# Optimization experiments

Hardware: AMD Instinct MI355X
Metric: run time of the kernel (lower is better)

## Reference

```python
import jax, jax.numpy as jnp
from jax import lax
import numpy as np

SEQ_LEN, INPUT_DIM, HID, NCLS, BATCH = 1024, 1, 512, 10, 256


def setup_inputs() -> dict:
    key = jax.random.key(0)
    k1, k2, k3, k4 = jax.random.split(key, 4)
    def xavier(k, shape):
        fan_in, fan_out = shape[1], shape[0]
        bound = np.sqrt(6.0 / (fan_in + fan_out))
        return jax.random.uniform(k, shape, jnp.float32, -bound, bound)
    return {
        "x": jax.random.normal(k1, (BATCH, SEQ_LEN), jnp.float32),
        "h_init": jnp.zeros((HID, 1), jnp.float32),
        "W_hx": xavier(k2, (HID, INPUT_DIM)),
        "W_hh": xavier(k3, (HID, HID)),
        "b_h": jnp.zeros((HID, 1), jnp.float32),
        "W_ph": xavier(k4, (NCLS, HID)),
        "b_p": jnp.zeros((NCLS, 1), jnp.float32),
    }


def reference(x, h_init, W_hx, W_hh, b_h, W_ph, b_p):
    # x: [B, T] scalar inputs per step (input_dim == 1)
    B = x.shape[0]
    H = h_init.shape[0]
    # Broadcasting h_init [H,1] to [H,B] up-front is mathematically identical
    # to the torch code (W_hh @ h_init broadcasts against [H,B] at step 0).
    h0 = jnp.broadcast_to(h_init, (H, B))

    def step(h, x_t):
        # x_t: [B]; W_hx @ x_t[None,:] -> [H, B]
        h_new = jnp.tanh(W_hx @ x_t[None, :] + W_hh @ h + b_h)
        return h_new, None

    h_last, _ = lax.scan(step, h0, x.T)  # scan over time axis [T, B]
    p = W_ph @ h_last + b_p  # [NCLS, B]
    return p.T  # [B, NCLS]
```

## Files before the change

kernel.cpp:

```cpp
#include <hip/hip_runtime.h>


#define T_SEQ    1024
#define HID      512
#define NTHREADS 512
#define NW       8
#define NCLS     10
#define RP       8
#define PAIRS    32
#define PREG     28
#define PSTRIDE  576

typedef _Float16 half2_t __attribute__((ext_vector_type(2)));

__device__ __forceinline__ unsigned int pack2(float a, float b) {
    half2_t h = {(_Float16)a, (_Float16)b};
    return __builtin_bit_cast(unsigned int, h);
}

__device__ __forceinline__ float dot2(unsigned int w, unsigned int h, float acc) {
#if __has_builtin(__builtin_amdgcn_fdot2)
    return __builtin_amdgcn_fdot2(__builtin_bit_cast(half2_t, w),
                                  __builtin_bit_cast(half2_t, h), acc, false);
#else
    half2_t wv = __builtin_bit_cast(half2_t, w), hv = __builtin_bit_cast(half2_t, h);
    return acc + (float)wv.x * (float)hv.x + (float)wv.y * (float)hv.y;
#endif
}

__device__ __forceinline__ unsigned int bcast(unsigned int v, int lane) {
#if __has_builtin(__builtin_amdgcn_readlane)
    return __builtin_amdgcn_readlane(v, lane);
#else
    return __shfl((int)v, lane, 64);
#endif
}

__device__ __forceinline__ int pidx(int row) { return row + ((row >> 5) << 2); }

__device__ __forceinline__ float fast_tanh(float s) {
#if __has_builtin(__builtin_amdgcn_exp2f)
    float e = __builtin_amdgcn_exp2f(s * 2.885390081777927f);
#else
    float e = __expf(2.0f * s);
#endif
    return 1.0f - 2.0f / (e + 1.0f);
}

__global__ __attribute__((amdgpu_flat_work_group_size(NTHREADS, NTHREADS)))
           __attribute__((amdgpu_waves_per_eu(2, 2)))
void rnn_persist(
    const float* __restrict__ x, const float* __restrict__ h_init,
    const float* __restrict__ W_hx, const float* __restrict__ W_hh,
    const float* __restrict__ b_h, const float* __restrict__ W_ph,
    const float* __restrict__ b_p, float* __restrict__ out)
{
    __shared__ uint4    Wl4[NW * RP * 64];
    __shared__ float    part[2][NW][PSTRIDE];
    __shared__ float    x_s[T_SEQ];
    __shared__ _Float16 hs[HID];

    const int tid  = threadIdx.x;
    const int b    = blockIdx.x;
    const int w    = tid >> 6;
    const int lane = tid & 63;

    for (int i = tid; i < T_SEQ; i += NTHREADS) x_s[i] = x[(size_t)b * T_SEQ + i];

    const float whx = W_hx[tid];
    const float bh  = b_h[tid];
    const int   pi  = pidx(tid);
    hs[tid] = (_Float16)h_init[tid];

    unsigned int wreg[RP][PREG];
    #pragma unroll
    for (int r = 0; r < RP; ++r) {
        const float4* row = (const float4*)(W_hh + (size_t)(RP * lane + r) * HID + 64 * w);
        #pragma unroll
        for (int q = 0; q < 7; ++q) {
            float4 v = row[q];
            wreg[r][2 * q]     = pack2(v.x, v.y);
            wreg[r][2 * q + 1] = pack2(v.z, v.w);
        }
#if __has_builtin(__builtin_amdgcn_sched_barrier)
        __builtin_amdgcn_sched_barrier(0);
#endif
        #pragma unroll
        for (int q = 7; q < 14; ++q) {
            float4 v = row[q];
            wreg[r][2 * q]     = pack2(v.x, v.y);
            wreg[r][2 * q + 1] = pack2(v.z, v.w);
        }
        float4 v14 = row[14], v15 = row[15];
        Wl4[(w * RP + r) * 64 + lane] =
            make_uint4(pack2(v14.x, v14.y), pack2(v14.z, v14.w),
                       pack2(v15.x, v15.y), pack2(v15.z, v15.w));
#if __has_builtin(__builtin_amdgcn_sched_barrier)
        __builtin_amdgcn_sched_barrier(0);
#endif
    }

    #pragma unroll
    for (int r = 0; r < RP; ++r)
        #pragma unroll
        for (int p = 0; p < PREG; ++p)
            asm volatile("" : "+v"(wreg[r][p]));

    __syncthreads();

    const unsigned int* hs32 = (const unsigned int*)hs;
    float hval = 0.0f;

    #pragma unroll 1
    for (int t = 0; t < T_SEQ; ++t) {
        const int buf = t & 1;
        const float xw = x_s[t];

        unsigned int hpack = hs32[w * 32 + (lane & 31)];

        float acc[RP];
        #pragma unroll
        for (int r = 0; r < RP; ++r) acc[r] = 0.0f;

        #pragma unroll
        for (int p = 0; p < PREG; ++p) {
            unsigned int hp = bcast(hpack, p);
            #pragma unroll
            for (int r = 0; r < RP; ++r) acc[r] = dot2(wreg[r][p], hp, acc[r]);
        }
        {
            unsigned int hh0 = bcast(hpack, 28), hh1 = bcast(hpack, 29),
                         hh2 = bcast(hpack, 30), hh3 = bcast(hpack, 31);
            #pragma unroll
            for (int r = 0; r < RP; ++r) {
                uint4 wq = Wl4[(w * RP + r) * 64 + lane];
                acc[r] = dot2(wq.x, hh0, acc[r]);
                acc[r] = dot2(wq.y, hh1, acc[r]);
                acc[r] = dot2(wq.z, hh2, acc[r]);
                acc[r] = dot2(wq.w, hh3, acc[r]);
            }
        }

        *(float4*)&part[buf][w][pidx(RP * lane)]     = make_float4(acc[0], acc[1], acc[2], acc[3]);
        *(float4*)&part[buf][w][pidx(RP * lane + 4)] = make_float4(acc[4], acc[5], acc[6], acc[7]);

        __syncthreads();

        float s = whx * xw + bh;
        #pragma unroll
        for (int j = 0; j < NW; ++j) s += part[buf][j][pi];

        hval = fast_tanh(s);
        hs[tid] = (_Float16)hval;
    }

    __syncthreads();
    x_s[tid] = hval;
    __syncthreads();

    for (int c = w; c < NCLS; c += NW) {
        float s = 0.0f;
        #pragma unroll
        for (int j = 0; j < 8; ++j) {
            int r = lane + 64 * j;
            s += W_ph[c * HID + r] * x_s[r];
        }
        #pragma unroll
        for (int off = 32; off; off >>= 1) s += __shfl_down(s, off, 64);
        if (lane == 0) out[b * NCLS + c] = s + b_p[c];
    }
}

extern "C" void kernel_launch(void* const* d_in, const int* in_sizes, int n_in,
                              void* d_out, int out_size, void* d_ws, size_t ws_size,
                              hipStream_t stream) {
    const float* x      = (const float*)d_in[0];
    const float* h_init = (const float*)d_in[1];
    const float* W_hx   = (const float*)d_in[2];
    const float* W_hh   = (const float*)d_in[3];
    const float* b_h    = (const float*)d_in[4];
    const float* W_ph   = (const float*)d_in[5];
    const float* b_p    = (const float*)d_in[6];
    float* out = (float*)d_out;

    const int B = in_sizes[0] / T_SEQ;
    rnn_persist<<<B, NTHREADS, 0, stream>>>(x, h_init, W_hx, W_hh, b_h, W_ph, b_p, out);
}
```

Before: 1.436 ms.

## Keep packed hidden state in registers, removing LDS h round-trip per step

Each lane now computes the two hidden rows that its wave will broadcast, using float2 reads of the partial sums, and packs the result directly into the register used for readlane broadcasts. This removes the per-step LDS write and read of the fp16 hidden vector, and with it the dependency on a second barrier. In exchange, both half-waves do redundant tanh and reduction work for duplicate rows, and the reduce now performs two tanh per lane.

```diff
diff --git a/kernel.cpp b/kernel.cpp
--- a/kernel.cpp
+++ b/kernel.cpp
@@ -55,22 +55,22 @@
     const float* __restrict__ b_h, const float* __restrict__ W_ph,
     const float* __restrict__ b_p, float* __restrict__ out)
 {
-    __shared__ uint4    Wl4[NW * RP * 64];
-    __shared__ float    part[2][NW][PSTRIDE];
-    __shared__ float    x_s[T_SEQ];
-    __shared__ _Float16 hs[HID];
+    __shared__ uint4 Wl4[NW * RP * 64];
+    __shared__ float part[2][NW][PSTRIDE];
+    __shared__ float x_s[T_SEQ];
 
     const int tid  = threadIdx.x;
     const int b    = blockIdx.x;
     const int w    = tid >> 6;
     const int lane = tid & 63;
+    const int p    = lane & 31;
 
     for (int i = tid; i < T_SEQ; i += NTHREADS) x_s[i] = x[(size_t)b * T_SEQ + i];
 
-    const float whx = W_hx[tid];
-    const float bh  = b_h[tid];
-    const int   pi  = pidx(tid);
-    hs[tid] = (_Float16)h_init[tid];
+    const int   R0   = 64 * w + 2 * p;
+    const float whx0 = W_hx[R0],     bh0 = b_h[R0];
+    const float whx1 = W_hx[R0 + 1], bh1 = b_h[R0 + 1];
+    const int   pi2  = pidx(2 * (32 * w + p));
 
     unsigned int wreg[RP][PREG];
     #pragma unroll
@@ -103,30 +103,28 @@
     #pragma unroll
     for (int r = 0; r < RP; ++r)
         #pragma unroll
-        for (int p = 0; p < PREG; ++p)
-            asm volatile("" : "+v"(wreg[r][p]));
+        for (int q = 0; q < PREG; ++q)
+            asm volatile("" : "+v"(wreg[r][q]));
 
     __syncthreads();
 
-    const unsigned int* hs32 = (const unsigned int*)hs;
-    float hval = 0.0f;
+    float h0 = h_init[R0], h1 = h_init[R0 + 1];
+    unsigned int hpack = pack2(h0, h1);
 
     #pragma unroll 1
     for (int t = 0; t < T_SEQ; ++t) {
         const int buf = t & 1;
         const float xw = x_s[t];
 
-        unsigned int hpack = hs32[w * 32 + (lane & 31)];
-
         float acc[RP];
         #pragma unroll
         for (int r = 0; r < RP; ++r) acc[r] = 0.0f;
 
         #pragma unroll
-        for (int p = 0; p < PREG; ++p) {
-            unsigned int hp = bcast(hpack, p);
+        for (int q = 0; q < PREG; ++q) {
+            unsigned int hp = bcast(hpack, q);
             #pragma unroll
-            for (int r = 0; r < RP; ++r) acc[r] = dot2(wreg[r][p], hp, acc[r]);
+            for (int r = 0; r < RP; ++r) acc[r] = dot2(wreg[r][q], hp, acc[r]);
         }
         {
             unsigned int hh0 = bcast(hpack, 28), hh1 = bcast(hpack, 29),
@@ -146,16 +144,24 @@
 
         __syncthreads();
 
-        float s = whx * xw + bh;
+        float s0 = whx0 * xw + bh0;
+        float s1 = whx1 * xw + bh1;
         #pragma unroll
-        for (int j = 0; j < NW; ++j) s += part[buf][j][pi];
-
-        hval = fast_tanh(s);
-        hs[tid] = (_Float16)hval;
+        for (int j = 0; j < NW; ++j) {
+            float2 pv = *(const float2*)&part[buf][j][pi2];
+            s0 += pv.x;
+            s1 += pv.y;
+        }
+        h0 = fast_tanh(s0);
+        h1 = fast_tanh(s1);
+        hpack = pack2(h0, h1);
     }
 
     __syncthreads();
-    x_s[tid] = hval;
+    if (lane < 32) {
+        x_s[R0]     = h0;
+        x_s[R0 + 1] = h1;
+    }
     __syncthreads();
 
     for (int c = w; c < NCLS; c += NW) {
```

New measurement: 1.639 ms. 1.14x slower.
